# Kernel optimization log

Hardware: AMD Instinct MI355X
Metric: run time of the kernel (lower is better)

Reference implementation:

```python
import jax, jax.numpy as jnp
import numpy as np

B, C, H, W = 16, 512, 112, 112
OUT, GMM = 8, 4
SIGMA_RATIO = 1.0
R = 3.0
BN_EPS = 1e-5


def conv3(x, w):
    # 3x3 conv, stride 1, padding 1 (SAME), NCHW / OIHW
    return jax.lax.conv_general_dilated(x, w, (1, 1), 'SAME',
                                        dimension_numbers=('NCHW', 'OIHW', 'NCHW'))


def bn_relu(x, g, b):
    # inference-mode BatchNorm2d (running_mean=0, running_var=1) + ReLU
    s = g / jnp.sqrt(1.0 + BN_EPS)
    return jax.nn.relu(x * s[None, :, None, None] + b[None, :, None, None])


def setup_inputs() -> dict:
    key = jax.random.key(0)
    ks = jax.random.split(key, 20)
    def w(k, shape, s=0.05):
        return jax.random.normal(k, shape, dtype=jnp.float32) * s
    inp = {
        'x':  jax.random.normal(ks[0], (B, C, H, W), dtype=jnp.float32),
        'w1': w(ks[1], (C // 2, C, 3, 3)),
        'g1': 1.0 + w(ks[2], (C // 2,), 0.1), 'b1': w(ks[3], (C // 2,), 0.1),
        'w2': w(ks[4], (C // 2, C // 2, 3, 3)),
        'g2': 1.0 + w(ks[5], (C // 2,), 0.1), 'b2': w(ks[6], (C // 2,), 0.1),
        'w3': w(ks[7], (C // 4, C // 2, 3, 3)),
        'g3': 1.0 + w(ks[8], (C // 4,), 0.1), 'b3': w(ks[9], (C // 4,), 0.1),
        'w4': w(ks[10], (C // 4, C // 4, 3, 3)),
        'g4': 1.0 + w(ks[11], (C // 4,), 0.1), 'b4': w(ks[12], (C // 4,), 0.1),
        'w5': w(ks[13], (C // 8, C // 4, 3, 3)),
        'g5': 1.0 + w(ks[14], (C // 8,), 0.1), 'b5': w(ks[15], (C // 8,), 0.1),
        'w_fc': w(ks[16], (4 * GMM * OUT, 9 * C // 8)),
        'mix_w': jnp.zeros((1, OUT, GMM, 1, 1), dtype=jnp.float32),
    }
    return inp


def reference(x, w1, g1, b1, w2, g2, b2, w3, g3, b3, w4, g4, b4, w5, g5, b5,
              w_fc, mix_w):
    Bn, Cn, Hh, Ww = x.shape
    h = bn_relu(conv3(x, w1), g1, b1)
    h = bn_relu(conv3(h, w2), g2, b2)
    # AdaptiveAvgPool2d((7,7)): 112/7 = 16, exact reshape-mean
    h = h.reshape(Bn, Cn // 2, 7, Hh // 7, 7, Ww // 7).mean(axis=(3, 5))
    h = bn_relu(conv3(h, w3), g3, b3)
    h = bn_relu(conv3(h, w4), g4, b4)
    # AdaptiveAvgPool2d((3,3)) on 7x7: overlapping windows size 3, stride 2
    h = jax.lax.reduce_window(h, 0.0, jax.lax.add, (1, 1, 3, 3), (1, 1, 2, 2), 'VALID') / 9.0
    h = bn_relu(conv3(h, w5), g5, b5)        # [B, C/8, 3, 3]
    feats = h.reshape(Bn, -1) @ w_fc.T       # [B, 4*gmm*out]
    f = feats.reshape(Bn, OUT, GMM, 4)

    H2, W2 = Hh // 2, Ww // 2
    m_x = jax.nn.sigmoid(f[..., 0]) * float(H2 - 1)           # [B,out,gmm]
    m_y = jax.nn.sigmoid(f[..., 1]) * float(W2 - 1)
    r = jnp.exp((jax.nn.sigmoid(f[..., 2]) * 2.0 - 1.0) * np.float32(np.log(R)))
    rho = jax.nn.sigmoid(f[..., 3]) * 1.6 - 0.8
    sigma = float(Hh) / (2.0 * SIGMA_RATIO)
    denom = -0.5 / (1.0 - rho ** 2) / (sigma ** 2)            # [B,out,gmm]

    ii = jnp.arange(H2, dtype=x.dtype)
    jj = jnp.arange(W2, dtype=x.dtype)
    dx = m_x[..., None] - ii   # [B,out,gmm,H2]
    dy = m_y[..., None] - jj   # [B,out,gmm,W2]
    quad = (dx ** 2 * r[..., None])[..., :, None] \
         + (dy ** 2 / r[..., None])[..., None, :] \
         - 2.0 * rho[..., None, None] * dx[..., :, None] * dy[..., None, :]
    att = jnp.exp(denom[..., None, None] * quad)              # [B,out,gmm,H2,W2]
    att = att / att.sum(axis=(3, 4), keepdims=True)
    mw = jax.nn.softmax(mix_w, axis=2)                        # [1,out,gmm,1,1]
    return (att * mw).sum(axis=2)                             # [B,out,H2,W2]
```

## Files before the change

### kernel.cpp

```cpp
#include <hip/hip_runtime.h>
#include <math.h>


typedef __attribute__((ext_vector_type(8))) short short8v;
typedef __attribute__((ext_vector_type(4))) float f32x4;

__device__ __forceinline__ void split_bf16(float f, unsigned int& hi, unsigned int& lo)
{
    unsigned int u = __float_as_uint(f);
    hi = u >> 16;
    float hif = __uint_as_float(u & 0xffff0000u);
    lo = __float_as_uint(f - hif) >> 16;
}

__device__ __forceinline__ void gld16(const void* g, void* l)
{
    __builtin_amdgcn_global_load_lds(
        (const __attribute__((address_space(1))) unsigned int*)g,
        (__attribute__((address_space(3))) unsigned int*)l, 16, 0, 0);
}

__global__ void zero_kernel(float* z) { z[threadIdx.x] = 0.f; }

__global__ __launch_bounds__(256)
void prep_w_kernel(const float* __restrict__ w, unsigned short* __restrict__ wp, int CIN)
{
    int idx = blockIdx.x * 256 + threadIdx.x;
    int NCH = CIN >> 5;
    int total = 2 * NCH * 9 * 2 * 128 * 32;
    if (idx >= total) return;
    int kk = idx & 31;
    int co = (idx >> 5) & 127;
    int pl = (idx >> 12) & 1;
    int rest = idx >> 13;
    int tap = rest % 9;
    rest /= 9;
    int ch = rest % NCH;
    int y = rest / NCH;
    int qp = kk >> 3, e = kk & 7;
    int q = qp ^ ((co >> 1) & 3);
    int ci = ch * 32 + q * 8 + e;
    int cog = y * 128 + co;
    float f = w[((size_t)cog * CIN + ci) * 9 + tap];
    unsigned int hi, lo;
    split_bf16(f, hi, lo);
    wp[idx] = (unsigned short)(pl ? lo : hi);
}

__global__ __launch_bounds__(256)
void presplit_x_kernel(const float* __restrict__ x, unsigned short* __restrict__ xs)
{
    const int gy = blockIdx.x, ch = blockIdx.y, b = blockIdx.z;
    const int tid = threadIdx.x;
    __shared__ float s[32][113];
    for (int i = tid; i < 32 * 112; i += 256) {
        int ci = i / 112, xx = i - ci * 112;
        s[ci][xx] = x[(((size_t)(b * 16 + ch) * 32 + ci) * 112 + gy) * 112 + xx];
    }
    __syncthreads();
    unsigned int* oh = (unsigned int*)(xs + ((size_t)(b * 16 + ch) * 2 * 12544 + (size_t)gy * 112) * 32);
    unsigned int* ol = oh + 12544 * 16;
    for (int i = tid; i < 112 * 16; i += 256) {
        int px = i >> 4, t = i & 15;
        int qp = t >> 2, ep = t & 3;
        int sw = ((18 * gy + px + 19) >> 1) & 3;
        int q = qp ^ sw;
        int ci0 = q * 8 + ep * 2;
        float f0 = s[ci0][px], f1 = s[ci0 + 1][px];
        unsigned int h0, l0, h1, l1;
        split_bf16(f0, h0, l0);
        split_bf16(f1, h1, l1);
        oh[(size_t)px * 16 + t] = h0 | (h1 << 16);
        ol[(size_t)px * 16 + t] = l0 | (l1 << 16);
    }
}

template<int CIN, bool POOL>
__global__ __launch_bounds__(256, 2)
void conv_mfma_kernel(const unsigned short* __restrict__ xs,
                      const unsigned short* __restrict__ wp,
                      const float* __restrict__ gam, const float* __restrict__ bet,
                      void* __restrict__ out_, const float* __restrict__ zerob)
{
    constexpr int NCH = CIN >> 5;
    __shared__ __align__(16) char sA[43008];
    __shared__ __align__(16) char sB[16384];

    const int tid = threadIdx.x;
    const int lane = tid & 63;
    const int wv = tid >> 6;
    const int wvm = wv >> 1, ng = wv & 1;
    const int m = lane & 15, kg = lane >> 4;
    const int ty = blockIdx.x / 7, tx = blockIdx.x % 7;
    const int yb = blockIdx.y;
    const int b = blockIdx.z;

    int aoff[11];
    unsigned adst[11];
    #pragma unroll
    for (int k2 = 0; k2 < 11; ++k2) {
        int j = wv + 4 * k2;
        aoff[k2] = -1; adst[k2] = 0;
        if (j < 42) {
            int pl = j / 21, jj = j - pl * 21;
            int px = jj * 16 + (lane >> 2);
            int py = px / 18, pxx = px - py * 18;
            int gy = ty * 16 + py - 1, gx = tx * 16 + pxx - 1;
            bool valid = (px < 324) && ((unsigned)gy < 112u) && ((unsigned)gx < 112u);
            aoff[k2] = valid ? (pl * 802816 + ((gy * 112 + gx) << 6) + ((lane & 3) << 4)) : -1;
            adst[k2] = pl * 21504 + jj * 1024;
        }
    }
    const char* zb = (const char*)zerob + ((lane & 3) << 4);

    auto issueA = [&](int ch) {
        const char* xbase = (const char*)xs + (size_t)(b * NCH + ch) * 1605632;
        #pragma unroll
        for (int k2 = 0; k2 < 11; ++k2) {
            if (wv + 4 * k2 < 42) {
                const char* g = (aoff[k2] >= 0) ? (xbase + aoff[k2]) : zb;
                gld16(g, sA + adst[k2]);
            }
        }
    };
    const char* wbase = (const char*)wp + (size_t)yb * ((size_t)NCH * 9 * 16384);
    auto issueB = [&](int flat) {
        const char* gb = wbase + (size_t)flat * 16384 + (wv << 12) + (lane << 4);
        #pragma unroll
        for (int j2 = 0; j2 < 4; ++j2)
            gld16(gb + j2 * 1024, sB + (wv << 12) + j2 * 1024);
    };

    f32x4 acc[8][4];
    #pragma unroll
    for (int i = 0; i < 8; ++i)
        #pragma unroll
        for (int j = 0; j < 4; ++j)
            acc[i][j] = (f32x4){0.f, 0.f, 0.f, 0.f};

    issueA(0);
    issueB(0);
    asm volatile("s_waitcnt vmcnt(0)" ::: "memory");
    __syncthreads();

    for (int ch = 0; ch < NCH; ++ch) {
        #pragma unroll
        for (int tap = 0; tap < 9; ++tap) {
            const int ky = tap / 3, kx = tap % 3;
            short8v Bf[8];
            #pragma unroll
            for (int nf = 0; nf < 4; ++nf) {
                int col = ng * 64 + nf * 16 + m;
                int off = col * 64 + ((kg ^ ((col >> 1) & 3)) << 4);
                Bf[nf * 2 + 0] = *(const short8v*)(sB + off);
                Bf[nf * 2 + 1] = *(const short8v*)(sB + 8192 + off);
            }
            #pragma unroll
            for (int mf = 0; mf < 8; ++mf) {
                int ap = (wvm * 8 + mf + ky) * 18 + kx + m;
                int off = ap * 64 + ((kg ^ ((ap >> 1) & 3)) << 4);
                short8v Ah = *(const short8v*)(sA + off);
                short8v Al = *(const short8v*)(sA + 21504 + off);
                #pragma unroll
                for (int nf = 0; nf < 4; ++nf) {
                    acc[mf][nf] = __builtin_amdgcn_mfma_f32_16x16x32_bf16(Ah, Bf[nf * 2 + 0], acc[mf][nf], 0, 0, 0);
                    acc[mf][nf] = __builtin_amdgcn_mfma_f32_16x16x32_bf16(Ah, Bf[nf * 2 + 1], acc[mf][nf], 0, 0, 0);
                    acc[mf][nf] = __builtin_amdgcn_mfma_f32_16x16x32_bf16(Al, Bf[nf * 2 + 0], acc[mf][nf], 0, 0, 0);
                }
            }
            __syncthreads();
            int flat = ch * 9 + tap + 1;
            if (flat < NCH * 9) issueB(flat);
            if (tap == 8 && ch + 1 < NCH) issueA(ch + 1);
            asm volatile("s_waitcnt vmcnt(0)" ::: "memory");
            __syncthreads();
        }
    }

    const float kRS = 1.0f / sqrtf(1.0f + 1e-5f);

    if (!POOL) {
        unsigned short* h1s = (unsigned short*)out_;
        #pragma unroll
        for (int mf = 0; mf < 8; ++mf) {
            int gy = ty * 16 + wvm * 8 + mf;
            #pragma unroll
            for (int nf = 0; nf < 4; ++nf) {
                int co = yb * 128 + ng * 64 + nf * 16 + m;
                float sc = gam[co] * kRS, bi = bet[co];
                int ch2 = co >> 5, sl = co & 31, q = sl >> 3, e = sl & 7;
                size_t base = (size_t)(b * 8 + ch2) * 802816;
                #pragma unroll
                for (int r = 0; r < 4; ++r) {
                    int gx = tx * 16 + kg * 4 + r;
                    float v = fmaxf(fmaf(acc[mf][nf][r], sc, bi), 0.f);
                    unsigned int hi, lo;
                    split_bf16(v, hi, lo);
                    int sw = ((18 * gy + gx + 19) >> 1) & 3;
                    size_t po = base + ((size_t)gy * 112 + gx) * 32 + (size_t)((q ^ sw) * 8 + e);
                    h1s[po] = (unsigned short)hi;
                    h1s[po + 401408] = (unsigned short)lo;
                }
            }
        }
    } else {
        __syncthreads();
        float* spool = (float*)sB;
        #pragma unroll
        for (int nf = 0; nf < 4; ++nf) {
            int co = yb * 128 + ng * 64 + nf * 16 + m;
            float sc = gam[co] * kRS, bi = bet[co];
            float s = 0.f;
            #pragma unroll
            for (int mf = 0; mf < 8; ++mf)
                #pragma unroll
                for (int r = 0; r < 4; ++r)
                    s += fmaxf(fmaf(acc[mf][nf][r], sc, bi), 0.f);
            s += __shfl_xor(s, 16);
            s += __shfl_xor(s, 32);
            if (lane < 16) spool[wv * 64 + nf * 16 + m] = s;
        }
        __syncthreads();
        if (tid < 128) {
            int ngx = tid >> 6, cl = tid & 63;
            float s = spool[ngx * 64 + cl] + spool[(2 + ngx) * 64 + cl];
            float* p1o = (float*)out_;
            p1o[(((size_t)b * 256 + yb * 128 + ngx * 64 + cl) * 7 + ty) * 7 + tx] = s * (1.f / 256.f);
        }
    }
}


template<int CIN>
__global__ __launch_bounds__(256)
void conv_small_kernel(const float* __restrict__ in, const float* __restrict__ w,
                       const float* __restrict__ gam, const float* __restrict__ bet,
                       float* __restrict__ out, int CO_TOT)
{
    const int co0 = blockIdx.x * 16;
    const int b = blockIdx.y;
    const int tid = threadIdx.x;
    const int px = tid & 63;
    const int wg = tid >> 6;
    const int py = px / 7, pxx = px - py * 7;
    const bool act = px < 49;

    __shared__ float s_in[64][9][9];
    __shared__ float s_w[64][16][9];

    float acc[4] = {0.f, 0.f, 0.f, 0.f};

    for (int ci0 = 0; ci0 < CIN; ci0 += 64) {
        __syncthreads();
        for (int idx = tid; idx < 64 * 81; idx += 256) {
            int ci = idx / 81;
            int rem = idx - ci * 81;
            int r = rem / 9, c = rem - (rem / 9) * 9;
            float v = 0.f;
            if (r >= 1 && r <= 7 && c >= 1 && c <= 7)
                v = in[((size_t)(b * CIN + ci0 + ci) * 7 + (r - 1)) * 7 + (c - 1)];
            s_in[ci][r][c] = v;
        }
        for (int idx = tid; idx < 64 * 16 * 9; idx += 256) {
            int co = idx / 576;
            int rem = idx - co * 576;
            int ci = rem / 9, tap = rem - (rem / 9) * 9;
            s_w[ci][co][tap] = w[((size_t)(co0 + co) * CIN + ci0 + ci) * 9 + tap];
        }
        __syncthreads();
        if (act) {
            for (int ci = 0; ci < 64; ++ci) {
                #pragma unroll
                for (int ky = 0; ky < 3; ++ky)
                    #pragma unroll
                    for (int kx = 0; kx < 3; ++kx) {
                        float v = s_in[ci][py + ky][pxx + kx];
                        #pragma unroll
                        for (int j = 0; j < 4; ++j)
                            acc[j] = fmaf(v, s_w[ci][wg * 4 + j][ky * 3 + kx], acc[j]);
                    }
            }
        }
    }
    if (act) {
        const float kRS = 1.0f / sqrtf(1.0f + 1e-5f);
        #pragma unroll
        for (int j = 0; j < 4; ++j) {
            int cog = co0 + wg * 4 + j;
            float v = fmaxf(fmaf(acc[j], gam[cog] * kRS, bet[cog]), 0.f);
            out[(size_t)(b * CO_TOT + cog) * 49 + py * 7 + pxx] = v;
        }
    }
}

__global__ void pool3x3_kernel(const float* __restrict__ in, float* __restrict__ out)
{
    int o = blockIdx.x * 256 + threadIdx.x;
    if (o >= 16 * 128 * 9) return;
    int xo = o % 3;
    int yo = (o / 3) % 3;
    int bc = o / 9;
    const float* p = in + (size_t)bc * 49;
    float s = 0.f;
    #pragma unroll
    for (int ky = 0; ky < 3; ++ky)
        #pragma unroll
        for (int kx = 0; kx < 3; ++kx)
            s += p[(yo * 2 + ky) * 7 + xo * 2 + kx];
    out[o] = s * (1.0f / 9.0f);
}

__global__ __launch_bounds__(256)
void conv5_kernel(const float* __restrict__ in, const float* __restrict__ w,
                  const float* __restrict__ gam, const float* __restrict__ bet,
                  float* __restrict__ out)
{
    const int co0 = blockIdx.x * 16;
    const int b = blockIdx.y;
    const int tid = threadIdx.x;
    __shared__ float s_in[128][5][5];
    __shared__ float s_w[64][16][9];

    for (int idx = tid; idx < 128 * 25; idx += 256) {
        int ci = idx / 25;
        int rem = idx - ci * 25;
        int r = rem / 5, c = rem - (rem / 5) * 5;
        float v = 0.f;
        if (r >= 1 && r <= 3 && c >= 1 && c <= 3)
            v = in[((size_t)(b * 128 + ci) * 3 + (r - 1)) * 3 + (c - 1)];
        s_in[ci][r][c] = v;
    }

    float acc = 0.f;
    const int co = tid / 9;
    const int px = tid - co * 9;
    const int pyy = px / 3, pxx = px - pyy * 3;
    const bool act = tid < 144;

    for (int ci0 = 0; ci0 < 128; ci0 += 64) {
        __syncthreads();
        for (int idx = tid; idx < 64 * 16 * 9; idx += 256) {
            int c2 = idx / 576;
            int rem = idx - c2 * 576;
            int ci = rem / 9, tap = rem - (rem / 9) * 9;
            s_w[ci][c2][tap] = w[((size_t)(co0 + c2) * 128 + ci0 + ci) * 9 + tap];
        }
        __syncthreads();
        if (act) {
            for (int ci = 0; ci < 64; ++ci) {
                #pragma unroll
                for (int ky = 0; ky < 3; ++ky)
                    #pragma unroll
                    for (int kx = 0; kx < 3; ++kx)
                        acc = fmaf(s_in[ci0 + ci][pyy + ky][pxx + kx],
                                   s_w[ci][co][ky * 3 + kx], acc);
            }
        }
    }
    if (act) {
        const float kRS = 1.0f / sqrtf(1.0f + 1e-5f);
        int cog = co0 + co;
        out[(size_t)(b * 64 + cog) * 9 + px] =
            fmaxf(fmaf(acc, gam[cog] * kRS, bet[cog]), 0.f);
    }
}

__global__ void fc_kernel(const float* __restrict__ h5, const float* __restrict__ wfc,
                          float* __restrict__ feats)
{
    int o = blockIdx.x * 256 + threadIdx.x;
    if (o >= 16 * 128) return;
    int b = o >> 7, j = o & 127;
    const float* hp = h5 + b * 576;
    const float* wp = wfc + j * 576;
    float s = 0.f;
    for (int k = 0; k < 576; ++k) s = fmaf(hp[k], wp[k], s);
    feats[o] = s;
}

__global__ __launch_bounds__(256)
void attn_kernel(const float* __restrict__ feats, const float* __restrict__ mixw,
                 float* __restrict__ out)
{
    const int bo = blockIdx.x;
    const int b = bo >> 3, o = bo & 7;
    const int tid = threadIdx.x;
    __shared__ float s_att[4][3136];
    __shared__ float s_red[4];

    float mv[4];
    float mmax = -1e30f;
    #pragma unroll
    for (int g = 0; g < 4; ++g) { mv[g] = mixw[o * 4 + g]; mmax = fmaxf(mmax, mv[g]); }
    float msum = 0.f;
    #pragma unroll
    for (int g = 0; g < 4; ++g) { mv[g] = expf(mv[g] - mmax); msum += mv[g]; }
    #pragma unroll
    for (int g = 0; g < 4; ++g) mv[g] /= msum;

    const float LOG_R = 1.0986122886681098f;
    float winv[4];
    for (int g = 0; g < 4; ++g) {
        float f0 = feats[b * 128 + o * 16 + g * 4 + 0];
        float f1 = feats[b * 128 + o * 16 + g * 4 + 1];
        float f2 = feats[b * 128 + o * 16 + g * 4 + 2];
        float f3 = feats[b * 128 + o * 16 + g * 4 + 3];
        float m_x = 55.f / (1.f + expf(-f0));
        float m_y = 55.f / (1.f + expf(-f1));
        float r = expf((2.f / (1.f + expf(-f2)) - 1.f) * LOG_R);
        float rho = 1.6f / (1.f + expf(-f3)) - 0.8f;
        float denom = (-0.5f / (1.f - rho * rho)) * (1.f / 3136.f);
        float rin = 1.f / r;

        float ssum = 0.f;
        for (int p = tid; p < 3136; p += 256) {
            int i = p / 56;
            int j = p - i * 56;
            float dx = m_x - (float)i;
            float dy = m_y - (float)j;
            float quad = dx * dx * r + dy * dy * rin - 2.f * rho * dx * dy;
            float e = expf(denom * quad);
            s_att[g][p] = e;
            ssum += e;
        }
        #pragma unroll
        for (int off = 32; off > 0; off >>= 1) ssum += __shfl_down(ssum, off);
        if ((tid & 63) == 0) s_red[tid >> 6] = ssum;
        __syncthreads();
        winv[g] = mv[g] / (s_red[0] + s_red[1] + s_red[2] + s_red[3]);
        __syncthreads();
    }

    for (int p = tid; p < 3136; p += 256) {
        float v = 0.f;
        #pragma unroll
        for (int g = 0; g < 4; ++g) v += s_att[g][p] * winv[g];
        out[(size_t)bo * 3136 + p] = v;
    }
}


extern "C" void kernel_launch(void* const* d_in, const int* in_sizes, int n_in,
                              void* d_out, int out_size, void* d_ws, size_t ws_size,
                              hipStream_t stream)
{
    const float* x    = (const float*)d_in[0];
    const float* w1   = (const float*)d_in[1];
    const float* g1   = (const float*)d_in[2];
    const float* b1   = (const float*)d_in[3];
    const float* w2   = (const float*)d_in[4];
    const float* g2   = (const float*)d_in[5];
    const float* b2   = (const float*)d_in[6];
    const float* w3   = (const float*)d_in[7];
    const float* g3   = (const float*)d_in[8];
    const float* b3   = (const float*)d_in[9];
    const float* w4   = (const float*)d_in[10];
    const float* g4   = (const float*)d_in[11];
    const float* b4   = (const float*)d_in[12];
    const float* w5   = (const float*)d_in[13];
    const float* g5   = (const float*)d_in[14];
    const float* b5   = (const float*)d_in[15];
    const float* wfc  = (const float*)d_in[16];
    const float* mixw = (const float*)d_in[17];
    float* outp = (float*)d_out;

    char* wsb = (char*)d_ws;
    unsigned short* wp = (unsigned short*)wsb;   wsb += (size_t)2359296 * 2;
    unsigned short* xs = (unsigned short*)wsb;   wsb += (size_t)16*16*2*12544*32*2;
    unsigned short* h1s = (unsigned short*)wsb;  wsb += (size_t)16*8*2*12544*32*2;
    float* p1 = (float*)wsb;  wsb += 200704 * 4;
    float* h3 = (float*)wsb;  wsb += 100352 * 4;
    float* h4 = (float*)wsb;  wsb += 100352 * 4;
    float* p2 = (float*)wsb;  wsb += 18432 * 4;
    float* h5 = (float*)wsb;  wsb += 9216 * 4;
    float* fts = (float*)wsb; wsb += 2048 * 4;
    float* zerob = (float*)wsb; wsb += 64 * 4;

    zero_kernel<<<1, 64, 0, stream>>>(zerob);
    presplit_x_kernel<<<dim3(112, 16, 16), 256, 0, stream>>>(x, xs);

    prep_w_kernel<<<9216, 256, 0, stream>>>(w1, wp, 512);
    conv_mfma_kernel<512, false><<<dim3(49, 2, 16), 256, 0, stream>>>(xs, wp, g1, b1, h1s, zerob);

    prep_w_kernel<<<4608, 256, 0, stream>>>(w2, wp, 256);
    conv_mfma_kernel<256, true><<<dim3(49, 2, 16), 256, 0, stream>>>(h1s, wp, g2, b2, p1, zerob);

    conv_small_kernel<256><<<dim3(8, 16), 256, 0, stream>>>(p1, w3, g3, b3, h3, 128);
    conv_small_kernel<128><<<dim3(8, 16), 256, 0, stream>>>(h3, w4, g4, b4, h4, 128);

    pool3x3_kernel<<<72, 256, 0, stream>>>(h4, p2);
    conv5_kernel<<<dim3(4, 16), 256, 0, stream>>>(p2, w5, g5, b5, h5);
    fc_kernel<<<8, 256, 0, stream>>>(h5, wfc, fts);
    attn_kernel<<<128, 256, 0, stream>>>(fts, mixw, outp);
}
```

Measured before the change: 1.939 ms.

## Double-buffer weight tiles in LDS and prefetch two taps ahead in conv

The MFMA conv kernel moves to dynamic shared memory with two weight-tile buffers. Weights for tap t+2 are now issued while tap t is computed, and the kernel waits only for the older load (vmcnt(4)) instead of draining every outstanding load each tap. s_setprio is raised around the MFMA block to favour compute waves. The cost is 16 KB more LDS per block, which could affect occupancy, and the input (A) reload at channel boundaries is still not overlapped.

```diff
diff --git a/kernel.cpp b/kernel.cpp
--- a/kernel.cpp
+++ b/kernel.cpp
@@ -83,8 +83,10 @@
                       void* __restrict__ out_, const float* __restrict__ zerob)
 {
     constexpr int NCH = CIN >> 5;
-    __shared__ __align__(16) char sA[43008];
-    __shared__ __align__(16) char sB[16384];
+    constexpr int NT = NCH * 9;
+    extern __shared__ __align__(16) char smem[];
+    char* sA = smem;
+    char* sB = smem + 43008;
 
     const int tid = threadIdx.x;
     const int lane = tid & 63;
@@ -124,11 +126,12 @@
         }
     };
     const char* wbase = (const char*)wp + (size_t)yb * ((size_t)NCH * 9 * 16384);
-    auto issueB = [&](int flat) {
+    auto issueB = [&](int flat, int buf) {
         const char* gb = wbase + (size_t)flat * 16384 + (wv << 12) + (lane << 4);
+        char* db = sB + buf * 16384 + (wv << 12);
         #pragma unroll
         for (int j2 = 0; j2 < 4; ++j2)
-            gld16(gb + j2 * 1024, sB + (wv << 12) + j2 * 1024);
+            gld16(gb + j2 * 1024, db + j2 * 1024);
     };
 
     f32x4 acc[8][4];
@@ -139,22 +142,27 @@
             acc[i][j] = (f32x4){0.f, 0.f, 0.f, 0.f};
 
     issueA(0);
-    issueB(0);
-    asm volatile("s_waitcnt vmcnt(0)" ::: "memory");
+    issueB(0, 0);
+    issueB(1, 1);
+    asm volatile("s_waitcnt vmcnt(4)" ::: "memory");
     __syncthreads();
 
     for (int ch = 0; ch < NCH; ++ch) {
         #pragma unroll
         for (int tap = 0; tap < 9; ++tap) {
+            const int t = ch * 9 + tap;
+            const int bsel = t & 1;
+            const char* sBc = sB + bsel * 16384;
             const int ky = tap / 3, kx = tap % 3;
             short8v Bf[8];
             #pragma unroll
             for (int nf = 0; nf < 4; ++nf) {
                 int col = ng * 64 + nf * 16 + m;
                 int off = col * 64 + ((kg ^ ((col >> 1) & 3)) << 4);
-                Bf[nf * 2 + 0] = *(const short8v*)(sB + off);
-                Bf[nf * 2 + 1] = *(const short8v*)(sB + 8192 + off);
-            }
+                Bf[nf * 2 + 0] = *(const short8v*)(sBc + off);
+                Bf[nf * 2 + 1] = *(const short8v*)(sBc + 8192 + off);
+            }
+            __builtin_amdgcn_s_setprio(1);
             #pragma unroll
             for (int mf = 0; mf < 8; ++mf) {
                 int ap = (wvm * 8 + mf + ky) * 18 + kx + m;
@@ -168,11 +176,16 @@
                     acc[mf][nf] = __builtin_amdgcn_mfma_f32_16x16x32_bf16(Al, Bf[nf * 2 + 0], acc[mf][nf], 0, 0, 0);
                 }
             }
+            __builtin_amdgcn_s_setprio(0);
             __syncthreads();
-            int flat = ch * 9 + tap + 1;
-            if (flat < NCH * 9) issueB(flat);
-            if (tap == 8 && ch + 1 < NCH) issueA(ch + 1);
-            asm volatile("s_waitcnt vmcnt(0)" ::: "memory");
+            if (tap == 8 && ch + 1 < NCH)
+                issueA(ch + 1);
+            if (t + 2 < NT) {
+                issueB(t + 2, bsel);
+                asm volatile("s_waitcnt vmcnt(4)" ::: "memory");
+            } else {
+                asm volatile("s_waitcnt vmcnt(0)" ::: "memory");
+            }
             __syncthreads();
         }
     }
@@ -205,7 +218,7 @@
         }
     } else {
         __syncthreads();
-        float* spool = (float*)sB;
+        float* spool = (float*)smem;
         #pragma unroll
         for (int nf = 0; nf < 4; ++nf) {
             int co = yb * 128 + ng * 64 + nf * 16 + m;
@@ -464,6 +477,11 @@
     const float* mixw = (const float*)d_in[17];
     float* outp = (float*)d_out;
 
+    hipFuncSetAttribute(reinterpret_cast<const void*>(&conv_mfma_kernel<512, false>),
+                        hipFuncAttributeMaxDynamicSharedMemorySize, 75776);
+    hipFuncSetAttribute(reinterpret_cast<const void*>(&conv_mfma_kernel<256, true>),
+                        hipFuncAttributeMaxDynamicSharedMemorySize, 75776);
+
     char* wsb = (char*)d_ws;
     unsigned short* wp = (unsigned short*)wsb;   wsb += (size_t)2359296 * 2;
     unsigned short* xs = (unsigned short*)wsb;   wsb += (size_t)16*16*2*12544*32*2;
@@ -480,10 +498,10 @@
     presplit_x_kernel<<<dim3(112, 16, 16), 256, 0, stream>>>(x, xs);
 
     prep_w_kernel<<<9216, 256, 0, stream>>>(w1, wp, 512);
-    conv_mfma_kernel<512, false><<<dim3(49, 2, 16), 256, 0, stream>>>(xs, wp, g1, b1, h1s, zerob);
+    conv_mfma_kernel<512, false><<<dim3(49, 2, 16), 256, 75776, stream>>>(xs, wp, g1, b1, h1s, zerob);
 
     prep_w_kernel<<<4608, 256, 0, stream>>>(w2, wp, 256);
-    conv_mfma_kernel<256, true><<<dim3(49, 2, 16), 256, 0, stream>>>(h1s, wp, g2, b2, p1, zerob);
+    conv_mfma_kernel<256, true><<<dim3(49, 2, 16), 256, 75776, stream>>>(h1s, wp, g2, b2, p1, zerob);
 
     conv_small_kernel<256><<<dim3(8, 16), 256, 0, stream>>>(p1, w3, g3, b3, h3, 128);
     conv_small_kernel<128><<<dim3(8, 16), 256, 0, stream>>>(h3, w4, g4, b4, h4, 128);
```

After: 2.663 ms. +37.4%, slower.

## Load conv weights directly into registers with prefetch, drop per-tap barriers

Applied to the files above, without the earlier changes.

The weight tile for each tap is no longer staged through LDS. Each lane now reads its B fragments straight from global memory into registers, double-buffered one tap ahead, and the weight prep no longer applies the LDS bank swizzle. This removes the two __syncthreads and the full vmcnt wait after every tap, leaving only one sync pair per 32-channel chunk when the activation tile is reloaded. The cost is more VGPR pressure, which could hurt occupancy at launch bounds of 2 blocks per SM, and exposed global-load latency if the one-tap prefetch is not enough to hide it.

```diff
diff --git a/kernel.cpp b/kernel.cpp
--- a/kernel.cpp
+++ b/kernel.cpp
@@ -37,9 +37,7 @@
     rest /= 9;
     int ch = rest % NCH;
     int y = rest / NCH;
-    int qp = kk >> 3, e = kk & 7;
-    int q = qp ^ ((co >> 1) & 3);
-    int ci = ch * 32 + q * 8 + e;
+    int ci = ch * 32 + kk;
     int cog = y * 128 + co;
     float f = w[((size_t)cog * CIN + ci) * 9 + tap];
     unsigned int hi, lo;
@@ -83,8 +81,8 @@
                       void* __restrict__ out_, const float* __restrict__ zerob)
 {
     constexpr int NCH = CIN >> 5;
+    constexpr int NT = NCH * 9;
     __shared__ __align__(16) char sA[43008];
-    __shared__ __align__(16) char sB[16384];
 
     const int tid = threadIdx.x;
     const int lane = tid & 63;
@@ -123,12 +121,17 @@
             }
         }
     };
-    const char* wbase = (const char*)wp + (size_t)yb * ((size_t)NCH * 9 * 16384);
-    auto issueB = [&](int flat) {
-        const char* gb = wbase + (size_t)flat * 16384 + (wv << 12) + (lane << 4);
-        #pragma unroll
-        for (int j2 = 0; j2 < 4; ++j2)
-            gld16(gb + j2 * 1024, sB + (wv << 12) + j2 * 1024);
+
+    const char* wbase = (const char*)wp + (size_t)yb * ((size_t)NCH * 9 * 16384)
+                        + ng * 4096 + m * 64 + kg * 16;
+    short8v Bh[4], Bl[4], Bh2[4], Bl2[4];
+    auto loadB = [&](int flat, short8v* BH, short8v* BL) {
+        const char* gb = wbase + (size_t)flat * 16384;
+        #pragma unroll
+        for (int nf = 0; nf < 4; ++nf) {
+            BH[nf] = *(const short8v*)(gb + nf * 1024);
+            BL[nf] = *(const short8v*)(gb + 8192 + nf * 1024);
+        }
     };
 
     f32x4 acc[8][4];
@@ -139,22 +142,16 @@
             acc[i][j] = (f32x4){0.f, 0.f, 0.f, 0.f};
 
     issueA(0);
-    issueB(0);
+    loadB(0, Bh, Bl);
     asm volatile("s_waitcnt vmcnt(0)" ::: "memory");
     __syncthreads();
 
     for (int ch = 0; ch < NCH; ++ch) {
         #pragma unroll
         for (int tap = 0; tap < 9; ++tap) {
+            const int flat = ch * 9 + tap;
+            if (flat + 1 < NT) loadB(flat + 1, Bh2, Bl2);
             const int ky = tap / 3, kx = tap % 3;
-            short8v Bf[8];
-            #pragma unroll
-            for (int nf = 0; nf < 4; ++nf) {
-                int col = ng * 64 + nf * 16 + m;
-                int off = col * 64 + ((kg ^ ((col >> 1) & 3)) << 4);
-                Bf[nf * 2 + 0] = *(const short8v*)(sB + off);
-                Bf[nf * 2 + 1] = *(const short8v*)(sB + 8192 + off);
-            }
             #pragma unroll
             for (int mf = 0; mf < 8; ++mf) {
                 int ap = (wvm * 8 + mf + ky) * 18 + kx + m;
@@ -163,18 +160,18 @@
                 short8v Al = *(const short8v*)(sA + 21504 + off);
                 #pragma unroll
                 for (int nf = 0; nf < 4; ++nf) {
-                    acc[mf][nf] = __builtin_amdgcn_mfma_f32_16x16x32_bf16(Ah, Bf[nf * 2 + 0], acc[mf][nf], 0, 0, 0);
-                    acc[mf][nf] = __builtin_amdgcn_mfma_f32_16x16x32_bf16(Ah, Bf[nf * 2 + 1], acc[mf][nf], 0, 0, 0);
-                    acc[mf][nf] = __builtin_amdgcn_mfma_f32_16x16x32_bf16(Al, Bf[nf * 2 + 0], acc[mf][nf], 0, 0, 0);
+                    acc[mf][nf] = __builtin_amdgcn_mfma_f32_16x16x32_bf16(Ah, Bh[nf], acc[mf][nf], 0, 0, 0);
+                    acc[mf][nf] = __builtin_amdgcn_mfma_f32_16x16x32_bf16(Ah, Bl[nf], acc[mf][nf], 0, 0, 0);
+                    acc[mf][nf] = __builtin_amdgcn_mfma_f32_16x16x32_bf16(Al, Bh[nf], acc[mf][nf], 0, 0, 0);
                 }
             }
-            __syncthreads();
-            int flat = ch * 9 + tap + 1;
-            if (flat < NCH * 9) issueB(flat);
-            if (tap == 8 && ch + 1 < NCH) issueA(ch + 1);
-            asm volatile("s_waitcnt vmcnt(0)" ::: "memory");
-            __syncthreads();
-        }
+            #pragma unroll
+            for (int nf = 0; nf < 4; ++nf) { Bh[nf] = Bh2[nf]; Bl[nf] = Bl2[nf]; }
+        }
+        __syncthreads();
+        if (ch + 1 < NCH) issueA(ch + 1);
+        asm volatile("s_waitcnt vmcnt(0)" ::: "memory");
+        __syncthreads();
     }
 
     const float kRS = 1.0f / sqrtf(1.0f + 1e-5f);
@@ -189,7 +186,7 @@
                 int co = yb * 128 + ng * 64 + nf * 16 + m;
                 float sc = gam[co] * kRS, bi = bet[co];
                 int ch2 = co >> 5, sl = co & 31, q = sl >> 3, e = sl & 7;
-                size_t base = (size_t)(b * 8 + ch2) * 802816;
+                size_t base2 = (size_t)(b * 8 + ch2) * 802816;
                 #pragma unroll
                 for (int r = 0; r < 4; ++r) {
                     int gx = tx * 16 + kg * 4 + r;
@@ -197,7 +194,7 @@
                     unsigned int hi, lo;
                     split_bf16(v, hi, lo);
                     int sw = ((18 * gy + gx + 19) >> 1) & 3;
-                    size_t po = base + ((size_t)gy * 112 + gx) * 32 + (size_t)((q ^ sw) * 8 + e);
+                    size_t po = base2 + ((size_t)gy * 112 + gx) * 32 + (size_t)((q ^ sw) * 8 + e);
                     h1s[po] = (unsigned short)hi;
                     h1s[po + 401408] = (unsigned short)lo;
                 }
@@ -205,7 +202,7 @@
         }
     } else {
         __syncthreads();
-        float* spool = (float*)sB;
+        float* spool = (float*)sA;
         #pragma unroll
         for (int nf = 0; nf < 4; ++nf) {
             int co = yb * 128 + ng * 64 + nf * 16 + m;
@@ -218,14 +215,15 @@
                     s += fmaxf(fmaf(acc[mf][nf][r], sc, bi), 0.f);
             s += __shfl_xor(s, 16);
             s += __shfl_xor(s, 32);
-            if (lane < 16) spool[wv * 64 + nf * 16 + m] = s;
+            if (lane < 16) spool[(wv * 4 + nf) * 16 + lane] = s;
         }
         __syncthreads();
         if (tid < 128) {
-            int ngx = tid >> 6, cl = tid & 63;
-            float s = spool[ngx * 64 + cl] + spool[(2 + ngx) * 64 + cl];
+            int ngx = tid >> 6, rem = tid & 63;
+            int nf = rem >> 4, mm = rem & 15;
+            float s = spool[(ngx * 4 + nf) * 16 + mm] + spool[((2 + ngx) * 4 + nf) * 16 + mm];
             float* p1o = (float*)out_;
-            p1o[(((size_t)b * 256 + yb * 128 + ngx * 64 + cl) * 7 + ty) * 7 + tx] = s * (1.f / 256.f);
+            p1o[(((size_t)b * 256 + yb * 128 + tid) * 7 + ty) * 7 + tx] = s * (1.f / 256.f);
         }
     }
 }
```

Measured after the change: 6.338 ms. 3.27x slower.
